# Kernel tuning notes

Measured on AMD Instinct MI355X. Metric: run time of the kernel, lower is better.

Reference implementation:

```python
import jax, jax.numpy as jnp
import numpy as np

E = 1024  # embedding_size
H = 16    # multi_head_num


def setup_inputs() -> dict:
    key = jax.random.key(0)
    ks = jax.random.split(key, 9)
    B, N = 4, 1024
    s = 1.0 / np.sqrt(E)
    return {
        "x": jax.random.normal(ks[0], (B, N, E), dtype=jnp.float32),
        "Wq": jax.random.normal(ks[1], (E, E), dtype=jnp.float32) * s,
        "bq": jax.random.normal(ks[2], (E,), dtype=jnp.float32) * 0.02,
        "Wk": jax.random.normal(ks[3], (E, E), dtype=jnp.float32) * s,
        "bk": jax.random.normal(ks[4], (E,), dtype=jnp.float32) * 0.02,
        "Wv": jax.random.normal(ks[5], (E, E), dtype=jnp.float32) * s,
        "bv": jax.random.normal(ks[6], (E,), dtype=jnp.float32) * 0.02,
        "Wo": jax.random.normal(ks[7], (E, E), dtype=jnp.float32) * s,
        "bo": jax.random.normal(ks[8], (E,), dtype=jnp.float32) * 0.02,
    }


def reference(x, Wq, bq, Wk, bk, Wv, bv, Wo, bo):
    B, N, _ = x.shape
    d = E // H

    def heads(y):  # [B,N,E] -> [B,H,N,d]
        return y.reshape(B, N, H, d).transpose(0, 2, 1, 3)

    q = heads(x @ Wq.T + bq)
    k = heads(x @ Wk.T + bk)
    v = heads(x @ Wv.T + bv)

    energy = jnp.einsum('bhqd,bhkd->bhqk', q, k)
    # NOTE: module divides by sqrt(E) AFTER softmax (faithful to source)
    scaling = jnp.asarray(E, x.dtype) ** 0.5
    att = jax.nn.softmax(energy, axis=-1) / scaling
    out = jnp.einsum('bhal,bhlv->bhav', att, v)
    out = out.transpose(0, 2, 1, 3).reshape(B, N, E)
    return out @ Wo.T + bo
```

## Files before the change

kernel.cpp:

```cpp
#include <hip/hip_runtime.h>
#include <hip/hip_bf16.h>


typedef __bf16 bf16x8 __attribute__((ext_vector_type(8)));
typedef __bf16 bf16x4 __attribute__((ext_vector_type(4)));
typedef float  f32x4  __attribute__((ext_vector_type(4)));

#define LOG2E 1.44269504f

__device__ __forceinline__ void glds16(const __bf16* g, __bf16* l) {
  __builtin_amdgcn_global_load_lds(
      (const __attribute__((address_space(1))) void*)g,
      (__attribute__((address_space(3))) void*)l, 16, 0, 0);
}

__global__ __launch_bounds__(256) void cvt_f32_bf16(const float* __restrict__ in,
                                                    __bf16* __restrict__ out, int n4) {
  int i = blockIdx.x * 256 + threadIdx.x;
  if (i < n4) {
    float4 v = *(const float4*)(in + (size_t)i * 4);
    bf16x4 b = {(__bf16)v.x, (__bf16)v.y, (__bf16)v.z, (__bf16)v.w};
    *(bf16x4*)(out + (size_t)i * 4) = b;
  }
}

__global__ __launch_bounds__(256) void cvt_all(const float* __restrict__ x,
                                               const float* __restrict__ Wq,
                                               const float* __restrict__ Wk,
                                               const float* __restrict__ Wv,
                                               const float* __restrict__ Wo,
                                               __bf16* __restrict__ xb,
                                               __bf16* __restrict__ Wqb,
                                               __bf16* __restrict__ Wkb,
                                               __bf16* __restrict__ Wvb,
                                               __bf16* __restrict__ Wob) {
  const int i = blockIdx.x * 256 + threadIdx.x;
  const float* src;
  __bf16* dst;
  int off;
  if (i < 1048576) {
    src = x; dst = xb; off = i;
  } else {
    const int j = i - 1048576;
    const int seg = j >> 18;
    off = j & 262143;
    src = (seg == 0) ? Wq : (seg == 1) ? Wk : (seg == 2) ? Wv : Wo;
    dst = (seg == 0) ? Wqb : (seg == 1) ? Wkb : (seg == 2) ? Wvb : Wob;
  }
  float4 v = *(const float4*)(src + (size_t)off * 4);
  bf16x4 b = {(__bf16)v.x, (__bf16)v.y, (__bf16)v.z, (__bf16)v.w};
  *(bf16x4*)(dst + (size_t)off * 4) = b;
}

template <bool WBF16>
__global__ __launch_bounds__(256, 3) void gemm_qkv(const __bf16* __restrict__ A,
                                                   const void* __restrict__ Wqp,
                                                   const void* __restrict__ Wkp,
                                                   const void* __restrict__ Wvp,
                                                   const float* __restrict__ bq,
                                                   const float* __restrict__ bk,
                                                   const float* __restrict__ bv,
                                                   __bf16* __restrict__ Qw,
                                                   __bf16* __restrict__ Kw,
                                                   __bf16* __restrict__ Vw) {
  constexpr int BST = WBF16 ? 64 : 72;
  __shared__ __attribute__((aligned(16))) __bf16 As[128][64];
  __shared__ __attribute__((aligned(16))) __bf16 Bs[128 * BST];

  const int tid = threadIdx.x;
  const int lane = tid & 63, w = tid >> 6;
  const int wm = w >> 1, wn = w & 1;
  const int l15 = lane & 15, lq = lane >> 4;
  const int lr = lane >> 3, lc = lane & 7;
  const int xs = l15 & 7;

  const int bid = blockIdx.x;
  const int c = bid & 7, t = bid >> 3;
  const int z = t >> 5;
  const int r = t & 31;
  const int nb = r & 7;
  const int mb = c * 4 + (r >> 3);
  const int m0 = mb * 128, n0 = nb * 128;

  const void* Wp = (z == 0) ? Wqp : (z == 1) ? Wkp : Wvp;
  const float* bias = (z == 0) ? bq : (z == 1) ? bk : bv;
  __bf16* C = (z == 0) ? Qw : (z == 1) ? Kw : Vw;
  const float scale = (z == 0) ? LOG2E : 1.0f;

  f32x4 acc[4][4] = {};

  for (int k0 = 0; k0 < 1024; k0 += 64) {
#pragma unroll
    for (int i = 0; i < 4; ++i) {
      const int row = w * 32 + i * 8 + lr;
      glds16(A + (size_t)(m0 + row) * 1024 + k0 + ((lc ^ lr) * 8), &As[row][lc * 8]);
    }
    if (WBF16) {
      const __bf16* Wb = (const __bf16*)Wp;
#pragma unroll
      for (int i = 0; i < 4; ++i) {
        const int row = w * 32 + i * 8 + lr;
        glds16(Wb + (size_t)(n0 + row) * 1024 + k0 + ((lc ^ lr) * 8), &Bs[row * 64 + lc * 8]);
      }
    } else {
      const float* W = (const float*)Wp;
#pragma unroll
      for (int i = 0; i < 8; ++i) {
        const int cc = i * 256 + tid, row = cc >> 4, col = (cc & 15) * 4;
        float4 wv = *(const float4*)(W + (size_t)(n0 + row) * 1024 + k0 + col);
        bf16x4 b4 = {(__bf16)wv.x, (__bf16)wv.y, (__bf16)wv.z, (__bf16)wv.w};
        *(bf16x4*)(&Bs[row * 72 + col]) = b4;
      }
    }
    __syncthreads();
#pragma unroll
    for (int s = 0; s < 2; ++s) {
      bf16x8 af[4], bfv[4];
#pragma unroll
      for (int mt = 0; mt < 4; ++mt)
        af[mt] = *(const bf16x8*)(&As[wm * 64 + mt * 16 + l15][((s * 4 + lq) ^ xs) * 8]);
#pragma unroll
      for (int nt = 0; nt < 4; ++nt) {
        const int row = wn * 64 + nt * 16 + l15;
        if (WBF16)
          bfv[nt] = *(const bf16x8*)(&Bs[row * 64 + (((s * 4 + lq) ^ xs) * 8)]);
        else
          bfv[nt] = *(const bf16x8*)(&Bs[row * 72 + s * 32 + lq * 8]);
      }
#pragma unroll
      for (int mt = 0; mt < 4; ++mt)
#pragma unroll
        for (int nt = 0; nt < 4; ++nt)
          acc[mt][nt] = __builtin_amdgcn_mfma_f32_16x16x32_bf16(
              af[mt], bfv[nt], acc[mt][nt], 0, 0, 0);
    }
    __syncthreads();
  }

#pragma unroll
  for (int mt = 0; mt < 4; ++mt) {
    const int mg_base = m0 + wm * 64 + mt * 16 + lq * 4;
    const int bb = mg_base >> 10, nr0 = mg_base & 1023;
#pragma unroll
    for (int nt = 0; nt < 4; ++nt) {
      const int ng = n0 + wn * 64 + nt * 16 + l15;
      const float bv = bias[ng];
      const int h = ng >> 6, dd = ng & 63;
      if (z != 2) {
#pragma unroll
        for (int rr = 0; rr < 4; ++rr) {
          const int mg = mg_base + rr;
          const size_t idx =
              ((size_t)(bb * 16 + h) << 16) + (size_t)(mg & 1023) * 64 + dd;
          C[idx] = (__bf16)((acc[mt][nt][rr] + bv) * scale);
        }
      } else {
        bf16x4 o4 = {(__bf16)(acc[mt][nt][0] + bv), (__bf16)(acc[mt][nt][1] + bv),
                     (__bf16)(acc[mt][nt][2] + bv), (__bf16)(acc[mt][nt][3] + bv)};
        *(bf16x4*)(&C[((size_t)(bb * 16 + h) << 16) + (size_t)dd * 1024 + nr0]) = o4;
      }
    }
  }
}

__global__ __launch_bounds__(256) void gemm_out(const __bf16* __restrict__ A,
                                                const __bf16* __restrict__ W,
                                                const float* __restrict__ bias,
                                                float* __restrict__ C) {
  __shared__ __attribute__((aligned(16))) __bf16 As[64][64];
  __shared__ __attribute__((aligned(16))) __bf16 Bs[128][64];

  const int tid = threadIdx.x;
  const int lane = tid & 63, w = tid >> 6;
  const int wm = w >> 1, wn = w & 1;
  const int l15 = lane & 15, lq = lane >> 4;
  const int lr = lane >> 3, lc = lane & 7;
  const int xs = l15 & 7;

  const int bid = blockIdx.x;
  const int c = bid & 7, t = bid >> 3;
  const int mb = c * 8 + (t & 7);
  const int nb = t >> 3;
  const int m0 = mb * 64, n0 = nb * 128;

  f32x4 acc[2][4] = {};

  for (int k0 = 0; k0 < 1024; k0 += 64) {
#pragma unroll
    for (int i = 0; i < 2; ++i) {
      const int row = w * 16 + i * 8 + lr;
      glds16(A + (size_t)(m0 + row) * 1024 + k0 + ((lc ^ lr) * 8), &As[row][lc * 8]);
    }
#pragma unroll
    for (int i = 0; i < 4; ++i) {
      const int row = w * 32 + i * 8 + lr;
      glds16(W + (size_t)(n0 + row) * 1024 + k0 + ((lc ^ lr) * 8), &Bs[row][lc * 8]);
    }
    __syncthreads();
#pragma unroll
    for (int s = 0; s < 2; ++s) {
      bf16x8 af[2], bfv[4];
#pragma unroll
      for (int mt = 0; mt < 2; ++mt)
        af[mt] = *(const bf16x8*)(&As[wm * 32 + mt * 16 + l15][((s * 4 + lq) ^ xs) * 8]);
#pragma unroll
      for (int nt = 0; nt < 4; ++nt)
        bfv[nt] = *(const bf16x8*)(&Bs[wn * 64 + nt * 16 + l15][((s * 4 + lq) ^ xs) * 8]);
#pragma unroll
      for (int mt = 0; mt < 2; ++mt)
#pragma unroll
        for (int nt = 0; nt < 4; ++nt)
          acc[mt][nt] = __builtin_amdgcn_mfma_f32_16x16x32_bf16(
              af[mt], bfv[nt], acc[mt][nt], 0, 0, 0);
    }
    __syncthreads();
  }

#pragma unroll
  for (int mt = 0; mt < 2; ++mt) {
    const int mg_base = m0 + wm * 32 + mt * 16 + lq * 4;
#pragma unroll
    for (int nt = 0; nt < 4; ++nt) {
      const int ng = n0 + wn * 64 + nt * 16 + l15;
      const float bv = bias[ng];
#pragma unroll
      for (int r = 0; r < 4; ++r)
        C[(size_t)(mg_base + r) * 1024 + ng] = acc[mt][nt][r] + bv;
    }
  }
}

__global__ __launch_bounds__(256) void attn_kernel(const __bf16* __restrict__ Q,
                                                   const __bf16* __restrict__ K,
                                                   const __bf16* __restrict__ Vt,
                                                   __bf16* __restrict__ O) {
  __shared__ __attribute__((aligned(16))) __bf16 Ks[2][64][64];
  __shared__ __attribute__((aligned(16))) __bf16 Vs[2][64][64];
  __shared__ __attribute__((aligned(16))) __bf16 PQ[9216];

  __bf16(*Qst)[64] = (__bf16(*)[64])PQ;
  __bf16(*Ps)[32][72] = (__bf16(*)[32][72])PQ;

  const int tid = threadIdx.x;
  const int lane = tid & 63, w = tid >> 6;
  const int l15 = lane & 15, lq = lane >> 4;
  const int lr = lane >> 3, lc = lane & 7;
  const int xs = l15 & 7;

  const int bh = blockIdx.x;
  const int qt = blockIdx.y;
  const __bf16* Qh = Q + (size_t)bh * 65536;
  const __bf16* Kh = K + (size_t)bh * 65536;
  const __bf16* Vh = Vt + (size_t)bh * 65536;

#pragma unroll
  for (int i = 0; i < 4; ++i) {
    const int row = w * 32 + i * 8 + lr;
    glds16(Qh + (size_t)(qt * 128 + row) * 64 + ((lc ^ lr) * 8), &Qst[row][lc * 8]);
  }
#pragma unroll
  for (int i = 0; i < 2; ++i) {
    const int row = w * 16 + i * 8 + lr;
    glds16(Kh + (size_t)row * 64 + ((lc ^ lr) * 8), &Ks[0][row][lc * 8]);
    glds16(Vh + (size_t)row * 1024 + ((lc ^ lr) * 8), &Vs[0][row][lc * 8]);
  }
  __syncthreads();
  bf16x8 bqr[2][2];
#pragma unroll
  for (int nq = 0; nq < 2; ++nq)
#pragma unroll
    for (int s = 0; s < 2; ++s)
      bqr[nq][s] = *(const bf16x8*)(&Qst[w * 32 + nq * 16 + l15][((s * 4 + lq) ^ xs) * 8]);
  __syncthreads();

  float l_run[2] = {0.0f, 0.0f};
  f32x4 oacc[2][4] = {};

  int buf = 0;
  for (int kb = 0; kb < 16; ++kb) {
    if (kb < 15) {
#pragma unroll
      for (int i = 0; i < 2; ++i) {
        const int row = w * 16 + i * 8 + lr;
        glds16(Kh + (size_t)(kb + 1) * 4096 + (size_t)row * 64 + ((lc ^ lr) * 8),
               &Ks[buf ^ 1][row][lc * 8]);
        glds16(Vh + (size_t)row * 1024 + (kb + 1) * 64 + ((lc ^ lr) * 8),
               &Vs[buf ^ 1][row][lc * 8]);
      }
    }

    f32x4 sacc[2][4] = {};
    __builtin_amdgcn_s_setprio(1);
#pragma unroll
    for (int s = 0; s < 2; ++s) {
#pragma unroll
      for (int mt = 0; mt < 4; ++mt) {
        bf16x8 ak = *(const bf16x8*)(&Ks[buf][mt * 16 + l15][((s * 4 + lq) ^ xs) * 8]);
#pragma unroll
        for (int nq = 0; nq < 2; ++nq)
          sacc[nq][mt] = __builtin_amdgcn_mfma_f32_16x16x32_bf16(
              ak, bqr[nq][s], sacc[nq][mt], 0, 0, 0);
      }
    }
    __builtin_amdgcn_s_setprio(0);

#pragma unroll
    for (int nq = 0; nq < 2; ++nq) {
      float sum = 0.0f;
#pragma unroll
      for (int mt = 0; mt < 4; ++mt)
#pragma unroll
        for (int r = 0; r < 4; ++r) {
          const float e = __builtin_amdgcn_exp2f(sacc[nq][mt][r]);
          sacc[nq][mt][r] = e;
          sum += e;
        }
      sum += __shfl_xor(sum, 16, 64);
      sum += __shfl_xor(sum, 32, 64);
      l_run[nq] += sum;
    }

#pragma unroll
    for (int nq = 0; nq < 2; ++nq)
#pragma unroll
      for (int mt = 0; mt < 4; ++mt) {
        bf16x4 p4 = {(__bf16)sacc[nq][mt][0], (__bf16)sacc[nq][mt][1],
                     (__bf16)sacc[nq][mt][2], (__bf16)sacc[nq][mt][3]};
        *(bf16x4*)(&Ps[w][nq * 16 + l15][mt * 16 + lq * 4]) = p4;
      }
    __threadfence_block();

    __builtin_amdgcn_s_setprio(1);
#pragma unroll
    for (int s = 0; s < 2; ++s) {
      bf16x8 bp[2];
#pragma unroll
      for (int nq = 0; nq < 2; ++nq)
        bp[nq] = *(const bf16x8*)(&Ps[w][nq * 16 + l15][s * 32 + lq * 8]);
#pragma unroll
      for (int mt = 0; mt < 4; ++mt) {
        bf16x8 av = *(const bf16x8*)(&Vs[buf][mt * 16 + l15][((s * 4 + lq) ^ xs) * 8]);
#pragma unroll
        for (int nq = 0; nq < 2; ++nq)
          oacc[nq][mt] = __builtin_amdgcn_mfma_f32_16x16x32_bf16(
              av, bp[nq], oacc[nq][mt], 0, 0, 0);
      }
    }
    __builtin_amdgcn_s_setprio(0);

    __syncthreads();
    buf ^= 1;
  }

  const int b = bh >> 4, h = bh & 15;
#pragma unroll
  for (int nq = 0; nq < 2; ++nq) {
    const float inv = 1.0f / (l_run[nq] * 32.0f);
    const size_t base =
        (size_t)(b * 1024 + qt * 128 + w * 32 + nq * 16 + l15) * 1024 + h * 64;
#pragma unroll
    for (int mt = 0; mt < 4; ++mt) {
      bf16x4 o4 = {(__bf16)(oacc[nq][mt][0] * inv), (__bf16)(oacc[nq][mt][1] * inv),
                   (__bf16)(oacc[nq][mt][2] * inv), (__bf16)(oacc[nq][mt][3] * inv)};
      *(bf16x4*)(&O[base + mt * 16 + lq * 4]) = o4;
    }
  }
}

extern "C" void kernel_launch(void* const* d_in, const int* in_sizes, int n_in,
                              void* d_out, int out_size, void* d_ws, size_t ws_size,
                              hipStream_t stream) {
  const float* x  = (const float*)d_in[0];
  const float* Wq = (const float*)d_in[1];
  const float* bq = (const float*)d_in[2];
  const float* Wk = (const float*)d_in[3];
  const float* bk = (const float*)d_in[4];
  const float* Wv = (const float*)d_in[5];
  const float* bv = (const float*)d_in[6];
  const float* Wo = (const float*)d_in[7];
  const float* bo = (const float*)d_in[8];
  float* out = (float*)d_out;

  const size_t SZ = (size_t)4 * 1024 * 1024;
  __bf16* Qw = (__bf16*)d_ws;
  __bf16* Kw = Qw + SZ;
  __bf16* Vw = Kw + SZ;
  __bf16* s3 = Vw + SZ;
  __bf16* xb = s3;
  __bf16* Ow = s3;

  dim3 blk(256);

  if (ws_size >= (size_t)40 * 1024 * 1024) {
    __bf16* Wqb = s3 + SZ;
    __bf16* Wkb = Wqb + SZ / 4;
    __bf16* Wvb = Wkb + SZ / 4;
    __bf16* Wob = Wvb + SZ / 4;
    cvt_all<<<8192, blk, 0, stream>>>(x, Wq, Wk, Wv, Wo, xb, Wqb, Wkb, Wvb, Wob);
    gemm_qkv<true><<<dim3(768), blk, 0, stream>>>(xb, Wqb, Wkb, Wvb,
                                                  bq, bk, bv, Qw, Kw, Vw);
    attn_kernel<<<dim3(64, 8), blk, 0, stream>>>(Qw, Kw, Vw, Ow);
    gemm_out<<<dim3(512), blk, 0, stream>>>(Ow, Wob, bo, out);
  } else {
    __bf16* Wob = Kw;
    cvt_f32_bf16<<<4096, blk, 0, stream>>>(x, xb, 1048576);
    gemm_qkv<false><<<dim3(768), blk, 0, stream>>>(xb, Wq, Wk, Wv,
                                                   bq, bk, bv, Qw, Kw, Vw);
    attn_kernel<<<dim3(64, 8), blk, 0, stream>>>(Qw, Kw, Vw, Ow);
    cvt_f32_bf16<<<1024, blk, 0, stream>>>(Wo, Wob, 262144);
    gemm_out<<<dim3(512), blk, 0, stream>>>(Ow, Wob, bo, out);
  }
}
```

Before: 164.1 us.

## Replace QKV GEMM with 256x256-tile, 8-wave, 4-stage LDS pipelined kernel

Adds a new QKV projection kernel that uses 512 threads per block and 256x256 output tiles, giving 192 blocks in place of 768. It stages tiles into a 4-slot, 128 KB dynamic LDS ring with direct global-to-LDS loads and XOR swizzling. Explicit vmcnt waits keep three stages in flight, and s_setprio is raised around the MFMA bursts. The larger tiles cut global traffic per FLOP, but fewer blocks and heavy LDS and register use may leave the GPU's CUs underfilled.

```diff
diff --git a/kernel.cpp b/kernel.cpp
--- a/kernel.cpp
+++ b/kernel.cpp
@@ -52,6 +52,140 @@
   *(bf16x4*)(dst + (size_t)off * 4) = b;
 }
 
+__global__ __launch_bounds__(512, 2) void gemm_qkv8(const __bf16* __restrict__ A,
+                                                    const __bf16* __restrict__ Wqp,
+                                                    const __bf16* __restrict__ Wkp,
+                                                    const __bf16* __restrict__ Wvp,
+                                                    const float* __restrict__ bq,
+                                                    const float* __restrict__ bk,
+                                                    const float* __restrict__ bv,
+                                                    __bf16* __restrict__ Qw,
+                                                    __bf16* __restrict__ Kw,
+                                                    __bf16* __restrict__ Vw) {
+  extern __shared__ __attribute__((aligned(16))) __bf16 lds[];
+
+  const int tid = threadIdx.x;
+  const int lane = tid & 63;
+  const int w = tid >> 6, wm = w >> 2, wn = w & 3;
+  const int l15 = lane & 15, lq = lane >> 4;
+
+  const int bid = blockIdx.x;
+  const int c = bid & 7, t = bid >> 3;
+  const int mb = c * 2 + (t & 1);
+  const int nb = t >> 1;
+  const int m0 = mb * 256;
+  const int n0g = nb * 256;
+  const int z = n0g >> 10;
+  const int n0l = n0g & 1023;
+
+  const __bf16* Wz = (z == 0) ? Wqp : (z == 1) ? Wkp : Wvp;
+  const float* bias = (z == 0) ? bq : (z == 1) ? bk : bv;
+  __bf16* C = (z == 0) ? Qw : (z == 1) ? Kw : Vw;
+  const float scale = (z == 0) ? LOG2E : 1.0f;
+
+  const int srow = tid >> 2;
+  const int scs = tid & 3;
+  const int sxor = (scs ^ (srow & 3)) * 8;
+  const __bf16* Asrc = A + (size_t)(m0 + srow) * 1024 + sxor;
+  const __bf16* Bsrc = Wz + (size_t)(n0l + srow) * 1024 + sxor;
+  __bf16* AsD = lds + (size_t)tid * 8;
+  __bf16* BsD = lds + 32768 + (size_t)tid * 8;
+
+#define STAGE_A(slot, kk)                                            \
+  do {                                                               \
+    glds16(Asrc + (kk), AsD + (slot) * 8192);                        \
+    glds16(Asrc + (kk) + 131072, AsD + (slot) * 8192 + 4096);        \
+  } while (0)
+#define STAGE_B(slot, kk)                                            \
+  do {                                                               \
+    glds16(Bsrc + (kk), BsD + (slot) * 8192);                        \
+    glds16(Bsrc + (kk) + 131072, BsD + (slot) * 8192 + 4096);        \
+  } while (0)
+
+  const int axor = (lq ^ (l15 & 3)) * 8;
+  const __bf16* aBase = lds + (wm * 128 + l15) * 32 + axor;
+  const __bf16* bBase = lds + 32768 + (wn * 64 + l15) * 32 + axor;
+
+  f32x4 acc[8][4] = {};
+
+#pragma unroll
+  for (int s = 0; s < 3; ++s) {
+    STAGE_A(s, s * 32);
+    STAGE_B(s, s * 32);
+  }
+
+  for (int s = 0; s < 32; ++s) {
+    if (s <= 29)
+      asm volatile("s_waitcnt vmcnt(8)" ::: "memory");
+    else if (s == 30)
+      asm volatile("s_waitcnt vmcnt(4)" ::: "memory");
+    else
+      asm volatile("s_waitcnt vmcnt(0)" ::: "memory");
+    __builtin_amdgcn_s_barrier();
+
+    const int slot = s & 3;
+    const __bf16* ap = aBase + slot * 8192;
+    const __bf16* bp = bBase + slot * 8192;
+
+    if (s + 3 < 32) STAGE_A((s + 3) & 3, (s + 3) * 32);
+
+    bf16x8 bf[4], af[4];
+#pragma unroll
+    for (int nt = 0; nt < 4; ++nt) bf[nt] = *(const bf16x8*)(bp + nt * 512);
+#pragma unroll
+    for (int mt = 0; mt < 4; ++mt) af[mt] = *(const bf16x8*)(ap + mt * 512);
+    __builtin_amdgcn_s_setprio(1);
+#pragma unroll
+    for (int mt = 0; mt < 4; ++mt)
+#pragma unroll
+      for (int nt = 0; nt < 4; ++nt)
+        acc[mt][nt] = __builtin_amdgcn_mfma_f32_16x16x32_bf16(af[mt], bf[nt],
+                                                              acc[mt][nt], 0, 0, 0);
+    __builtin_amdgcn_s_setprio(0);
+
+    __builtin_amdgcn_s_barrier();
+
+    if (s + 3 < 32) STAGE_B((s + 3) & 3, (s + 3) * 32);
+#pragma unroll
+    for (int mt = 0; mt < 4; ++mt) af[mt] = *(const bf16x8*)(ap + (4 + mt) * 512);
+    __builtin_amdgcn_s_setprio(1);
+#pragma unroll
+    for (int mt = 0; mt < 4; ++mt)
+#pragma unroll
+      for (int nt = 0; nt < 4; ++nt)
+        acc[4 + mt][nt] = __builtin_amdgcn_mfma_f32_16x16x32_bf16(af[mt], bf[nt],
+                                                                  acc[4 + mt][nt], 0, 0, 0);
+    __builtin_amdgcn_s_setprio(0);
+  }
+#undef STAGE_A
+#undef STAGE_B
+
+#pragma unroll
+  for (int mt = 0; mt < 8; ++mt) {
+    const int mg_base = m0 + wm * 128 + mt * 16 + lq * 4;
+    const int bb = mg_base >> 10, nr0 = mg_base & 1023;
+#pragma unroll
+    for (int nt = 0; nt < 4; ++nt) {
+      const int nl = n0l + wn * 64 + nt * 16 + l15;
+      const float bv = bias[nl];
+      const int h = nl >> 6, dd = nl & 63;
+      if (z != 2) {
+#pragma unroll
+        for (int rr = 0; rr < 4; ++rr) {
+          const int mg = mg_base + rr;
+          const size_t idx =
+              ((size_t)(bb * 16 + h) << 16) + (size_t)(mg & 1023) * 64 + dd;
+          C[idx] = (__bf16)((acc[mt][nt][rr] + bv) * scale);
+        }
+      } else {
+        bf16x4 o4 = {(__bf16)(acc[mt][nt][0] + bv), (__bf16)(acc[mt][nt][1] + bv),
+                     (__bf16)(acc[mt][nt][2] + bv), (__bf16)(acc[mt][nt][3] + bv)};
+        *(bf16x4*)(&C[((size_t)(bb * 16 + h) << 16) + (size_t)dd * 1024 + nr0]) = o4;
+      }
+    }
+  }
+}
+
 template <bool WBF16>
 __global__ __launch_bounds__(256, 3) void gemm_qkv(const __bf16* __restrict__ A,
                                                    const void* __restrict__ Wqp,
@@ -396,9 +530,15 @@
     __bf16* Wkb = Wqb + SZ / 4;
     __bf16* Wvb = Wkb + SZ / 4;
     __bf16* Wob = Wvb + SZ / 4;
+    static bool attr_set = false;
+    if (!attr_set) {
+      (void)hipFuncSetAttribute((const void*)gemm_qkv8,
+                                hipFuncAttributeMaxDynamicSharedMemorySize, 131072);
+      attr_set = true;
+    }
     cvt_all<<<8192, blk, 0, stream>>>(x, Wq, Wk, Wv, Wo, xb, Wqb, Wkb, Wvb, Wob);
-    gemm_qkv<true><<<dim3(768), blk, 0, stream>>>(xb, Wqb, Wkb, Wvb,
-                                                  bq, bk, bv, Qw, Kw, Vw);
+    gemm_qkv8<<<dim3(192), dim3(512), 131072, stream>>>(xb, Wqb, Wkb, Wvb,
+                                                        bq, bk, bv, Qw, Kw, Vw);
     attn_kernel<<<dim3(64, 8), blk, 0, stream>>>(Qw, Kw, Vw, Ow);
     gemm_out<<<dim3(512), blk, 0, stream>>>(Ow, Wob, bo, out);
   } else {
```

Measured after the change: 176.8 us. 1.08x slower.
